# Kernel tuning notes

Hardware: AMD Instinct MI355X
Metric: run time of the kernel (lower is better)

Reference implementation:

```python
import jax, jax.numpy as jnp
import numpy as np

N = 100            # node_num
B = 8              # batch
H = 256            # node_feature_hidden_dim
FD, FL = 16, 16    # node_feature_dim, node_feature_len
OUT = 4            # edge_output_dim
E = N * (N - 1)    # 9900 directed edges (off-diagonal)
_off = np.ones((N, N)) - np.eye(N)
REC, SEND = np.where(_off)   # rel_rec one-hot rows = REC, rel_send = SEND
REC = jnp.asarray(REC, jnp.int32)
SEND = jnp.asarray(SEND, jnp.int32)
BN_EPS = 1e-5


def _mlp(x, w1, b1, w2, b2, g, beta):
    # Linear-ReLU-Linear-ReLU-BatchNorm1d (training-mode batch stats, dropout=0)
    h = jax.nn.relu(x @ w1 + b1)
    h = jax.nn.relu(h @ w2 + b2)
    b_, e_, f_ = h.shape
    hf = h.reshape(b_ * e_, f_)
    mu = hf.mean(0)
    var = hf.var(0)  # biased variance, as torch BN uses for normalization
    hn = (hf - mu) * jax.lax.rsqrt(var + BN_EPS) * g + beta
    return hn.reshape(b_, e_, f_)


def _node2edge(x):
    # gather form of rel_send @ x / rel_rec @ x, cat([senders, receivers])
    return jnp.concatenate([x[:, SEND, :], x[:, REC, :]], axis=2)


def _edge2node(x):
    # scatter form of rel_rec.T @ x; original divides by incoming.size(1) == N
    incoming = jnp.zeros((x.shape[0], N, x.shape[2]), x.dtype).at[:, REC, :].add(x)
    return incoming / N


def setup_inputs() -> dict:
    key = jax.random.key(0)
    ks = jax.random.split(key, 40)

    def rn(k, shape, s=0.05):
        return (jax.random.normal(k, shape) * s).astype(jnp.float32)

    inp = {
        'x': rn(ks[0], (B, N, FD, FL), 1.0),
        'h': rn(ks[1], (B, N, 8, 8), 1.0),
        't_nodes': N,
        't_edges': E,
        'nodes_mask': jnp.ones((N,), jnp.int32),
        'edges_mask': jnp.ones((E,), jnp.int32),
    }
    n_in = {'mlp1': FD * FL, 'mlp2': 2 * H, 'mlp3': H, 'mlp4': 3 * H}
    i = 2
    for name, nin in n_in.items():
        inp[name + '_w1'] = rn(ks[i], (nin, H)); i += 1
        inp[name + '_b1'] = jnp.full((H,), 0.1, jnp.float32)
        inp[name + '_w2'] = rn(ks[i], (H, H)); i += 1
        inp[name + '_b2'] = jnp.full((H,), 0.1, jnp.float32)
        inp[name + '_g'] = jnp.ones((H,), jnp.float32)
        inp[name + '_beta'] = jnp.zeros((H,), jnp.float32)
    inp['fc_w'] = rn(ks[i], (H, OUT)); i += 1
    inp['fc_b'] = jnp.full((OUT,), 0.1, jnp.float32)
    return inp


def reference(x, h, t_nodes, t_edges, nodes_mask, edges_mask,
              mlp1_w1, mlp1_b1, mlp1_w2, mlp1_b2, mlp1_g, mlp1_beta,
              mlp2_w1, mlp2_b1, mlp2_w2, mlp2_b2, mlp2_g, mlp2_beta,
              mlp3_w1, mlp3_b1, mlp3_w2, mlp3_b2, mlp3_g, mlp3_beta,
              mlp4_w1, mlp4_b1, mlp4_w2, mlp4_b2, mlp4_g, mlp4_beta,
              fc_w, fc_b):
    # h, t_nodes, t_edges, nodes_mask, edges_mask are unused by the original forward
    xx = x.reshape(x.shape[0], x.shape[1], -1).astype(jnp.float32)  # [B,N,FD*FL]
    xx = _mlp(xx, mlp1_w1, mlp1_b1, mlp1_w2, mlp1_b2, mlp1_g, mlp1_beta)  # [B,N,H]
    xe = _node2edge(xx)                                                   # [B,E,2H]
    xe = _mlp(xe, mlp2_w1, mlp2_b1, mlp2_w2, mlp2_b2, mlp2_g, mlp2_beta)  # [B,E,H]
    x_skip = xe
    xn = _edge2node(xe)                                                   # [B,N,H]
    xn = _mlp(xn, mlp3_w1, mlp3_b1, mlp3_w2, mlp3_b2, mlp3_g, mlp3_beta)
    xe2 = _node2edge(xn)                                                  # [B,E,2H]
    xc = jnp.concatenate([xe2, x_skip], axis=2)                           # [B,E,3H]
    xc = _mlp(xc, mlp4_w1, mlp4_b1, mlp4_w2, mlp4_b2, mlp4_g, mlp4_beta)  # [B,E,H]
    z_g = xc @ fc_w + fc_b                                                # [B,E,OUT]
    return z_g
```

## Files before the change

kernel.cpp:

```cpp
#include <hip/hip_runtime.h>
#include <hip/hip_bf16.h>

#define Nn 100
#define Bb 8
#define Hh 256
#define Ee 9900
#define RE 79200
#define RN 800
#define BN_EPS 1e-5f

typedef __attribute__((ext_vector_type(8))) unsigned short ushort8_t;
typedef __attribute__((ext_vector_type(4))) unsigned short ushort4_t;
typedef __attribute__((ext_vector_type(8))) short bf16x8;
typedef __attribute__((ext_vector_type(4))) float f32x4;

__device__ __forceinline__ float bf2f(unsigned short u){
  return __uint_as_float(((unsigned)u) << 16);
}
__device__ __forceinline__ unsigned short f2bf(float f){
  unsigned u = __float_as_uint(f);
  return (unsigned short)((u + 0x7fffu + ((u >> 16) & 1u)) >> 16);
}

__device__ __forceinline__ void affine_prologue(const float* __restrict__ stats,
    float cnt, const float* __restrict__ g, const float* __restrict__ beta,
    float* a, float* c, int tid){
  if (tid < 256){
    float inv = 1.0f / cnt;
    float mu  = stats[tid] * inv;
    float var = fmaxf(stats[256 + tid] * inv - mu * mu, 0.f);
    float aa  = g[tid] * rsqrtf(var + BN_EPS);
    a[tid] = aa;
    c[tid] = beta[tid] - mu * aa;
  }
}

__device__ __forceinline__ void affine_reg(const float* __restrict__ stats,
    float cnt, const float* __restrict__ g, const float* __restrict__ be,
    int cb, float4& av, float4& cv){
  float4 s = *(const float4*)(stats + cb);
  float4 q = *(const float4*)(stats + 256 + cb);
  float4 gg = *(const float4*)(g + cb);
  float4 bb = *(const float4*)(be + cb);
  float inv = 1.0f / cnt;
  float mx = s.x*inv, my = s.y*inv, mz = s.z*inv, mw = s.w*inv;
  av.x = gg.x * rsqrtf(fmaxf(q.x*inv - mx*mx, 0.f) + BN_EPS); cv.x = bb.x - mx*av.x;
  av.y = gg.y * rsqrtf(fmaxf(q.y*inv - my*my, 0.f) + BN_EPS); cv.y = bb.y - my*av.y;
  av.z = gg.z * rsqrtf(fmaxf(q.z*inv - mz*mz, 0.f) + BN_EPS); cv.z = bb.z - mz*av.z;
  av.w = gg.w * rsqrtf(fmaxf(q.w*inv - mw*mw, 0.f) + BN_EPS); cv.w = bb.w - mw*av.w;
}

__device__ __forceinline__ void gemm_f32(const float* IN, const float* __restrict__ W,
                                         float acc[8][4], int tr, int tc){
  for (int k = 0; k < 256; k += 4){
    float4 w0 = *(const float4*)(W + (size_t)(k+0)*256 + 4*tc);
    float4 w1 = *(const float4*)(W + (size_t)(k+1)*256 + 4*tc);
    float4 w2 = *(const float4*)(W + (size_t)(k+2)*256 + 4*tc);
    float4 w3 = *(const float4*)(W + (size_t)(k+3)*256 + 4*tc);
    #pragma unroll
    for (int rr = 0; rr < 8; rr++){
      float4 iv = *(const float4*)(IN + (tr*8+rr)*256 + k);
      acc[rr][0] += iv.x*w0.x + iv.y*w1.x + iv.z*w2.x + iv.w*w3.x;
      acc[rr][1] += iv.x*w0.y + iv.y*w1.y + iv.z*w2.y + iv.w*w3.y;
      acc[rr][2] += iv.x*w0.z + iv.y*w1.z + iv.z*w2.z + iv.w*w3.z;
      acc[rr][3] += iv.x*w0.w + iv.y*w1.w + iv.z*w2.w + iv.w*w3.w;
    }
  }
}

template<int KW>
__device__ __forceinline__ void mfma_gemm(const unsigned short* Alds,
    const unsigned short* __restrict__ Bf, f32x4 acc[2][4], int w, int lane){
  const int l15 = lane & 15, kg = lane >> 4;
  for (int ks = 0; ks < KW/32; ks++){
    int byte0 = ((l15*KW      + ks*32 + kg*8) * 2) ^ ((l15 & 7) << 4);
    int byte1 = (((16+l15)*KW + ks*32 + kg*8) * 2) ^ ((l15 & 7) << 4);
    bf16x8 a0 = *(const bf16x8*)((const char*)Alds + byte0);
    bf16x8 a1 = *(const bf16x8*)((const char*)Alds + byte1);
    const unsigned short* bp = Bf + ((size_t)(ks*16 + w*4)*64 + lane)*8;
    #pragma unroll
    for (int cf = 0; cf < 4; cf++){
      bf16x8 b = *(const bf16x8*)(bp + cf*64*8);
      acc[0][cf] = __builtin_amdgcn_mfma_f32_16x16x32_bf16(a0, b, acc[0][cf], 0,0,0);
      acc[1][cf] = __builtin_amdgcn_mfma_f32_16x16x32_bf16(a1, b, acc[1][cf], 0,0,0);
    }
  }
}

__device__ __forceinline__ void zero_acc(f32x4 acc[2][4]){
  #pragma unroll
  for (int i = 0; i < 2; i++)
    #pragma unroll
    for (int j = 0; j < 4; j++){
      f32x4 z = {0.f, 0.f, 0.f, 0.f};
      acc[i][j] = z;
    }
}

#define STATS_PUSH(statsp)                                   \
  __syncthreads();                                           \
  atomicAdd(&(statsp)[tid], red[tid]);                       \
  atomicAdd(&(statsp)[tid + 256], red[tid + 256]);

__global__ void k_wprep(const float* __restrict__ W, unsigned short* __restrict__ out,
                        int ktiles){
  int id = blockIdx.x * 256 + threadIdx.x;
  int total = ktiles * 16 * 64;
  if (id >= total) return;
  int lane = id & 63, tile = id >> 6;
  int tc = tile & 15, tk = tile >> 4;
  int kbase = tk*32 + (lane>>4)*8, col = tc*16 + (lane&15);
  ushort8_t o;
  #pragma unroll
  for (int j = 0; j < 8; j++) o[j] = f2bf(W[(size_t)(kbase+j)*256 + col]);
  *(ushort8_t*)(out + (size_t)id*8) = o;
}

__global__ __launch_bounds__(256,2) void k_mlp1(
    const float* __restrict__ x,
    const float* __restrict__ W1, const float* __restrict__ b1,
    const float* __restrict__ W2, const float* __restrict__ b2,
    float* __restrict__ h1, float* __restrict__ stats){
  __shared__ float IN[32*256];
  __shared__ float O1[32*256];
  __shared__ float red[512];
  int tid = threadIdx.x, tr = tid >> 6, tc = tid & 63;
  int r0 = blockIdx.x * 32;
  #pragma unroll
  for (int j = 0; j < 8; j++){
    int idx = tid*4 + j*1024;
    *(float4*)(IN + idx) = *(const float4*)(x + (size_t)r0*256 + idx);
  }
  red[tid] = 0.f; red[tid + 256] = 0.f;
  __syncthreads();
  float acc[8][4];
  #pragma unroll
  for (int rr = 0; rr < 8; rr++){ acc[rr][0]=acc[rr][1]=acc[rr][2]=acc[rr][3]=0.f; }
  gemm_f32(IN, W1, acc, tr, tc);
  {
    float4 bb = *(const float4*)(b1 + 4*tc);
    #pragma unroll
    for (int rr = 0; rr < 8; rr++){
      float4 o;
      o.x = fmaxf(acc[rr][0]+bb.x, 0.f);
      o.y = fmaxf(acc[rr][1]+bb.y, 0.f);
      o.z = fmaxf(acc[rr][2]+bb.z, 0.f);
      o.w = fmaxf(acc[rr][3]+bb.w, 0.f);
      *(float4*)(O1 + (tr*8+rr)*256 + 4*tc) = o;
    }
  }
  __syncthreads();
  #pragma unroll
  for (int rr = 0; rr < 8; rr++){ acc[rr][0]=acc[rr][1]=acc[rr][2]=acc[rr][3]=0.f; }
  gemm_f32(O1, W2, acc, tr, tc);
  {
    float4 bb = *(const float4*)(b2 + 4*tc);
    float ls0=0,ls1=0,ls2=0,ls3=0,lq0=0,lq1=0,lq2=0,lq3=0;
    #pragma unroll
    for (int rr = 0; rr < 8; rr++){
      float4 v;
      v.x = fmaxf(acc[rr][0]+bb.x, 0.f);
      v.y = fmaxf(acc[rr][1]+bb.y, 0.f);
      v.z = fmaxf(acc[rr][2]+bb.z, 0.f);
      v.w = fmaxf(acc[rr][3]+bb.w, 0.f);
      *(float4*)(h1 + ((size_t)(r0 + tr*8 + rr))*256 + 4*tc) = v;
      ls0+=v.x; lq0+=v.x*v.x; ls1+=v.y; lq1+=v.y*v.y;
      ls2+=v.z; lq2+=v.z*v.z; ls3+=v.w; lq3+=v.w*v.w;
    }
    atomicAdd(&red[4*tc+0], ls0); atomicAdd(&red[4*tc+1], ls1);
    atomicAdd(&red[4*tc+2], ls2); atomicAdd(&red[4*tc+3], ls3);
    atomicAdd(&red[256+4*tc+0], lq0); atomicAdd(&red[256+4*tc+1], lq1);
    atomicAdd(&red[256+4*tc+2], lq2); atomicAdd(&red[256+4*tc+3], lq3);
  }
  STATS_PUSH(stats)
}

__global__ __launch_bounds__(256,2) void k_nodepq(
    const float* __restrict__ hsrc, const float* __restrict__ stats,
    const float* __restrict__ g, const float* __restrict__ be,
    const float* __restrict__ W512,
    float* __restrict__ P, float* __restrict__ Q){
  __shared__ float IN[32*256];
  int tid = threadIdx.x, tr = tid >> 6, tc = tid & 63;
  int part = blockIdx.x / 25;
  int r0 = (blockIdx.x % 25) * 32;
  int cb = (tid*4) & 255;
  float4 av, cv;
  affine_reg(stats, (float)RN, g, be, cb, av, cv);
  #pragma unroll
  for (int j = 0; j < 8; j++){
    int idx = tid*4 + j*1024;
    int row = idx >> 8;
    float4 v = *(const float4*)(hsrc + (size_t)(r0+row)*256 + cb);
    float4 o;
    o.x = v.x*av.x + cv.x; o.y = v.y*av.y + cv.y;
    o.z = v.z*av.z + cv.z; o.w = v.w*av.w + cv.w;
    *(float4*)(IN + idx) = o;
  }
  __syncthreads();
  float acc[8][4];
  #pragma unroll
  for (int rr = 0; rr < 8; rr++){ acc[rr][0]=acc[rr][1]=acc[rr][2]=acc[rr][3]=0.f; }
  gemm_f32(IN, W512 + (size_t)part*65536, acc, tr, tc);
  float* out = part ? Q : P;
  #pragma unroll
  for (int rr = 0; rr < 8; rr++){
    float4 o; o.x=acc[rr][0]; o.y=acc[rr][1]; o.z=acc[rr][2]; o.w=acc[rr][3];
    *(float4*)(out + (size_t)(r0 + tr*8 + rr)*256 + 4*tc) = o;
  }
}

__global__ __launch_bounds__(256,6) void k_mlp2(
    const float* __restrict__ P2, const float* __restrict__ Q2,
    const float* __restrict__ b1,
    const unsigned short* __restrict__ W2f, const float* __restrict__ b2,
    unsigned short* __restrict__ h2, float* __restrict__ stats2){
  __shared__ unsigned short O1[32*256];
  __shared__ float red[512];
  int tid = threadIdx.x, w = tid >> 6, lane = tid & 63;
  int l15 = lane & 15, kg = lane >> 4;
  int r0 = blockIdx.x * 32;
  red[tid] = 0.f; red[tid + 256] = 0.f;
  {
    int cb = lane * 4;
    float4 bb = *(const float4*)(b1 + cb);
    #pragma unroll
    for (int rr = 0; rr < 8; rr++){
      int rl = w*8+rr, rg = r0 + rl;
      int b = rg / Ee, e = rg - b*Ee;
      int i = e / 99, kk = e - i*99;
      int snd = kk + (kk >= i);
      float4 pv = *(const float4*)(P2 + ((size_t)(b*Nn + snd))*256 + cb);
      float4 qv = *(const float4*)(Q2 + ((size_t)(b*Nn + i))*256 + cb);
      ushort4_t o;
      o[0] = f2bf(fmaxf(pv.x+qv.x+bb.x, 0.f));
      o[1] = f2bf(fmaxf(pv.y+qv.y+bb.y, 0.f));
      o[2] = f2bf(fmaxf(pv.z+qv.z+bb.z, 0.f));
      o[3] = f2bf(fmaxf(pv.w+qv.w+bb.w, 0.f));
      int byte = ((rl*256 + cb)*2) ^ ((rl&7)<<4);
      *(ushort4_t*)((char*)O1 + byte) = o;
    }
  }
  __syncthreads();
  f32x4 acc2[2][4];
  zero_acc(acc2);
  mfma_gemm<256>(O1, W2f, acc2, w, lane);
  {
    #pragma unroll
    for (int cf = 0; cf < 4; cf++){
      int col = w*64 + cf*16 + l15;
      float bb = b2[col];
      float ls = 0.f, lq = 0.f;
      #pragma unroll
      for (int rf = 0; rf < 2; rf++){
        #pragma unroll
        for (int r = 0; r < 4; r++){
          int row = rf*16 + kg*4 + r;
          float v = fmaxf(acc2[rf][cf][r] + bb, 0.f);
          h2[(size_t)(r0 + row)*256 + col] = f2bf(v);
          ls += v; lq += v*v;
        }
      }
      atomicAdd(&red[col], ls);
      atomicAdd(&red[256+col], lq);
    }
  }
  STATS_PUSH(stats2)
}

__global__ __launch_bounds__(256,4) void k_e2n(
    const unsigned short* __restrict__ h2, float* __restrict__ h3in){
  int m = blockIdx.x;
  int b = m / Nn, i = m - b*Nn;
  int c = threadIdx.x;
  const unsigned short* base = h2 + ((size_t)(b*Ee + i*99))*256 + c;
  float s = 0.f;
  #pragma unroll 4
  for (int j = 0; j < 99; j++) s += bf2f(base[(size_t)j*256]);
  h3in[(size_t)m*256 + c] = s;
}

__global__ __launch_bounds__(256,2) void k_mlp3(
    const float* __restrict__ h3in, const float* __restrict__ stats2,
    const float* __restrict__ g2, const float* __restrict__ be2,
    const float* __restrict__ W1, const float* __restrict__ b1,
    const float* __restrict__ W2, const float* __restrict__ b2,
    float* __restrict__ h3, float* __restrict__ stats3){
  __shared__ float IN[32*256];
  __shared__ float O1[32*256];
  __shared__ float red[512];
  __shared__ float ap[256], cp[256];
  int tid = threadIdx.x, tr = tid >> 6, lane = tid & 63, tc = lane;
  int r0 = blockIdx.x * 32;
  affine_prologue(stats2, (float)RE, g2, be2, ap, cp, tid);
  red[tid] = 0.f; red[tid + 256] = 0.f;
  __syncthreads();
  {
    int cb = lane * 4;
    float4 av = *(const float4*)(ap+cb), cv = *(const float4*)(cp+cb);
    #pragma unroll
    for (int rr = 0; rr < 8; rr++){
      int m = r0 + tr*8 + rr;
      float4 s = *(const float4*)(h3in + (size_t)m*256 + cb);
      float4 o;
      o.x = (s.x*av.x + 99.f*cv.x) * 0.01f;
      o.y = (s.y*av.y + 99.f*cv.y) * 0.01f;
      o.z = (s.z*av.z + 99.f*cv.z) * 0.01f;
      o.w = (s.w*av.w + 99.f*cv.w) * 0.01f;
      *(float4*)(IN + (tr*8+rr)*256 + cb) = o;
    }
  }
  __syncthreads();
  float acc[8][4];
  #pragma unroll
  for (int rr = 0; rr < 8; rr++){ acc[rr][0]=acc[rr][1]=acc[rr][2]=acc[rr][3]=0.f; }
  gemm_f32(IN, W1, acc, tr, tc);
  {
    float4 bb = *(const float4*)(b1 + 4*tc);
    #pragma unroll
    for (int rr = 0; rr < 8; rr++){
      float4 o;
      o.x = fmaxf(acc[rr][0]+bb.x, 0.f);
      o.y = fmaxf(acc[rr][1]+bb.y, 0.f);
      o.z = fmaxf(acc[rr][2]+bb.z, 0.f);
      o.w = fmaxf(acc[rr][3]+bb.w, 0.f);
      *(float4*)(O1 + (tr*8+rr)*256 + 4*tc) = o;
    }
  }
  __syncthreads();
  #pragma unroll
  for (int rr = 0; rr < 8; rr++){ acc[rr][0]=acc[rr][1]=acc[rr][2]=acc[rr][3]=0.f; }
  gemm_f32(O1, W2, acc, tr, tc);
  {
    float4 bb = *(const float4*)(b2 + 4*tc);
    float ls0=0,ls1=0,ls2=0,ls3=0,lq0=0,lq1=0,lq2=0,lq3=0;
    #pragma unroll
    for (int rr = 0; rr < 8; rr++){
      float4 v;
      v.x = fmaxf(acc[rr][0]+bb.x, 0.f);
      v.y = fmaxf(acc[rr][1]+bb.y, 0.f);
      v.z = fmaxf(acc[rr][2]+bb.z, 0.f);
      v.w = fmaxf(acc[rr][3]+bb.w, 0.f);
      *(float4*)(h3 + ((size_t)(r0 + tr*8 + rr))*256 + 4*tc) = v;
      ls0+=v.x; lq0+=v.x*v.x; ls1+=v.y; lq1+=v.y*v.y;
      ls2+=v.z; lq2+=v.z*v.z; ls3+=v.w; lq3+=v.w*v.w;
    }
    atomicAdd(&red[4*tc+0], ls0); atomicAdd(&red[4*tc+1], ls1);
    atomicAdd(&red[4*tc+2], ls2); atomicAdd(&red[4*tc+3], ls3);
    atomicAdd(&red[256+4*tc+0], lq0); atomicAdd(&red[256+4*tc+1], lq1);
    atomicAdd(&red[256+4*tc+2], lq2); atomicAdd(&red[256+4*tc+3], lq3);
  }
  STATS_PUSH(stats3)
}

__global__ __launch_bounds__(256,6) void k_mlp4(
    const unsigned short* __restrict__ h2,
    const float* __restrict__ stats2, const float* __restrict__ g2, const float* __restrict__ be2,
    const float* __restrict__ P4, const float* __restrict__ Q4,
    const float* __restrict__ b1,
    const unsigned short* __restrict__ Wsf,
    const unsigned short* __restrict__ W2f, const float* __restrict__ b2,
    unsigned short* __restrict__ h4, float* __restrict__ stats4){
  __shared__ unsigned short A[32*256];
  __shared__ float red[512];
  __shared__ int sIdx[32], rIdx[32];
  int tid = threadIdx.x, w = tid >> 6, lane = tid & 63;
  int l15 = lane & 15, kg = lane >> 4;
  int r0 = blockIdx.x * 32;
  red[tid] = 0.f; red[tid + 256] = 0.f;
  if (tid < 32){
    int rg = r0 + tid;
    int b = rg / Ee, e = rg - b*Ee;
    int i = e / 99, kk = e - i*99;
    int snd = kk + (kk >= i);
    sIdx[tid] = (b*Nn + snd)*256;
    rIdx[tid] = (b*Nn + i)*256;
  }
  {
    int cb = lane * 4;
    float4 av, cv;
    affine_reg(stats2, (float)RE, g2, be2, cb, av, cv);
    #pragma unroll
    for (int rr = 0; rr < 8; rr++){
      int rl = w*8+rr, rg = r0 + rl;
      ushort4_t hv = *(const ushort4_t*)(h2 + (size_t)rg*256 + cb);
      ushort4_t o;
      o[0]=f2bf(bf2f(hv[0])*av.x+cv.x);
      o[1]=f2bf(bf2f(hv[1])*av.y+cv.y);
      o[2]=f2bf(bf2f(hv[2])*av.z+cv.z);
      o[3]=f2bf(bf2f(hv[3])*av.w+cv.w);
      int byte = ((rl*256 + cb)*2) ^ ((rl&7)<<4);
      *(ushort4_t*)((char*)A + byte) = o;
    }
  }
  __syncthreads();
  f32x4 acc[2][4];
  zero_acc(acc);
  mfma_gemm<256>(A, Wsf, acc, w, lane);
  __syncthreads();
  unsigned short* O1 = A;
  {
    #pragma unroll
    for (int cf = 0; cf < 4; cf++){
      int col = w*64 + cf*16 + l15;
      float bb = b1[col];
      #pragma unroll
      for (int rf = 0; rf < 2; rf++){
        #pragma unroll
        for (int r = 0; r < 4; r++){
          int row = rf*16 + kg*4 + r;
          float v = acc[rf][cf][r] + P4[sIdx[row] + col] + Q4[rIdx[row] + col] + bb;
          v = fmaxf(v, 0.f);
          int byte = ((row*256 + col)*2) ^ ((row&7)<<4);
          *(unsigned short*)((char*)O1 + byte) = f2bf(v);
        }
      }
    }
  }
  __syncthreads();
  f32x4 acc2[2][4];
  zero_acc(acc2);
  mfma_gemm<256>(O1, W2f, acc2, w, lane);
  {
    #pragma unroll
    for (int cf = 0; cf < 4; cf++){
      int col = w*64 + cf*16 + l15;
      float bb = b2[col];
      float ls = 0.f, lq = 0.f;
      #pragma unroll
      for (int rf = 0; rf < 2; rf++){
        #pragma unroll
        for (int r = 0; r < 4; r++){
          int row = rf*16 + kg*4 + r;
          float v = fmaxf(acc2[rf][cf][r] + bb, 0.f);
          h4[(size_t)(r0 + row)*256 + col] = f2bf(v);
          ls += v; lq += v*v;
        }
      }
      atomicAdd(&red[col], ls);
      atomicAdd(&red[256+col], lq);
    }
  }
  STATS_PUSH(stats4)
}

__global__ __launch_bounds__(256,2) void k_out(
    const unsigned short* __restrict__ h4, const float* __restrict__ stats4,
    const float* __restrict__ g4, const float* __restrict__ be4,
    const float* __restrict__ fcw, const float* __restrict__ fcb,
    float* __restrict__ out){
  __shared__ unsigned short T[64*264];
  __shared__ float a4[256], c4[256], Wl[1024];
  int tid = threadIdx.x;
  affine_prologue(stats4, (float)RE, g4, be4, a4, c4, tid);
  #pragma unroll
  for (int j = 0; j < 4; j++){ int id = tid + j*256; Wl[id] = fcw[id]; }
  int r0 = blockIdx.x * 64;
  #pragma unroll
  for (int j = 0; j < 8; j++){
    int flat = tid + j*256;
    int rl = flat >> 5, cs = (flat & 31) * 8;
    ushort8_t v = {0,0,0,0,0,0,0,0};
    if (r0 + rl < RE) v = *(const ushort8_t*)(h4 + (size_t)(r0+rl)*256 + cs);
    *(ushort8_t*)(&T[rl*264 + cs]) = v;
  }
  __syncthreads();
  int row = tid >> 2, o = tid & 3;
  if (r0 + row < RE){
    float acc = fcb[o];
    for (int k = 0; k < 256; k += 8){
      ushort8_t iv = *(const ushort8_t*)(&T[row*264 + k]);
      #pragma unroll
      for (int kk = 0; kk < 8; kk++){
        float v = bf2f(iv[kk]) * a4[k+kk] + c4[k+kk];
        acc += v * Wl[(k+kk)*4 + o];
      }
    }
    out[(size_t)(r0+row)*4 + o] = acc;
  }
}

extern "C" void kernel_launch(void* const* d_in, const int* in_sizes, int n_in,
                              void* d_out, int out_size, void* d_ws, size_t ws_size,
                              hipStream_t stream){
  const float* x    = (const float*)d_in[0];
  const float* m1w1 = (const float*)d_in[6];  const float* m1b1 = (const float*)d_in[7];
  const float* m1w2 = (const float*)d_in[8];  const float* m1b2 = (const float*)d_in[9];
  const float* m1g  = (const float*)d_in[10]; const float* m1be = (const float*)d_in[11];
  const float* m2w1 = (const float*)d_in[12]; const float* m2b1 = (const float*)d_in[13];
  const float* m2w2 = (const float*)d_in[14]; const float* m2b2 = (const float*)d_in[15];
  const float* m2g  = (const float*)d_in[16]; const float* m2be = (const float*)d_in[17];
  const float* m3w1 = (const float*)d_in[18]; const float* m3b1 = (const float*)d_in[19];
  const float* m3w2 = (const float*)d_in[20]; const float* m3b2 = (const float*)d_in[21];
  const float* m3g  = (const float*)d_in[22]; const float* m3be = (const float*)d_in[23];
  const float* m4w1 = (const float*)d_in[24]; const float* m4b1 = (const float*)d_in[25];
  const float* m4w2 = (const float*)d_in[26]; const float* m4b2 = (const float*)d_in[27];
  const float* m4g  = (const float*)d_in[28]; const float* m4be = (const float*)d_in[29];
  const float* fcw  = (const float*)d_in[30]; const float* fcb  = (const float*)d_in[31];

  size_t need_bytes = 1435648ull * 4ull
                    + (2ull * (size_t)RE * 256ull + 3ull * 65536ull) * 2ull;
  if (ws_size < need_bytes) return;

  float* ws = (float*)d_ws;
  float* h1   = ws;
  float* h3   = ws + 204800;
  float* stats= ws + 409600;
  float* h3in = ws + 411648;
  float* P2   = ws + 616448;
  float* Q2   = ws + 821248;
  float* P4   = ws + 1026048;
  float* Q4   = ws + 1230848;
  unsigned short* h2  = (unsigned short*)(ws + 1435648);
  unsigned short* h4  = h2 + (size_t)RE * 256;
  unsigned short* w2b = h4 + (size_t)RE * 256;
  unsigned short* w4s = w2b + 65536;
  unsigned short* w4b = w4s + 65536;

  hipMemsetAsync(stats, 0, 2048 * sizeof(float), stream);

  k_wprep<<<(8*16*64)/256, 256, 0, stream>>>(m2w2, w2b, 8);
  k_wprep<<<(8*16*64)/256, 256, 0, stream>>>(m4w1 + (size_t)512*256, w4s, 8);
  k_wprep<<<(8*16*64)/256, 256, 0, stream>>>(m4w2, w4b, 8);

  k_mlp1<<<RN/32, 256, 0, stream>>>(x, m1w1, m1b1, m1w2, m1b2, h1, stats);
  k_nodepq<<<50, 256, 0, stream>>>(h1, stats, m1g, m1be, m2w1, P2, Q2);
  k_mlp2<<<RE/32, 256, 0, stream>>>(P2, Q2, m2b1, w2b, m2b2, h2, stats + 512);
  k_e2n<<<RN, 256, 0, stream>>>(h2, h3in);
  k_mlp3<<<RN/32, 256, 0, stream>>>(h3in, stats + 512, m2g, m2be,
                                    m3w1, m3b1, m3w2, m3b2, h3, stats + 1024);
  k_nodepq<<<50, 256, 0, stream>>>(h3, stats + 1024, m3g, m3be, m4w1, P4, Q4);
  k_mlp4<<<RE/32, 256, 0, stream>>>(h2, stats + 512, m2g, m2be,
                                    P4, Q4, m4b1, w4s, w4b, m4b2, h4, stats + 1536);
  k_out<<<(RE+63)/64, 256, 0, stream>>>(h4, stats + 1536, m4g, m4be,
                                        fcw, fcb, (float*)d_out);
}
```

Before: 513.9 us.

## Use 64-row edge tiles in MFMA kernels and store node projections in bf16

The edge MLP kernels (mlp2, mlp4) now process 64 rows per block instead of 32, so each weight fragment loaded from global memory feeds four MFMA row-fragments rather than two. Tail rows are clamped on load and skipped on store. The node projections P/Q are also stored as bf16 instead of fp32, which halves the gather traffic in the edge kernels. In exchange, register and LDS use go up (launch bounds drop to 4 blocks), the grid shrinks, and there is a small loss of precision on P/Q.

```diff
diff --git a/kernel.cpp b/kernel.cpp
--- a/kernel.cpp
+++ b/kernel.cpp
@@ -68,28 +68,30 @@
   }
 }
 
-template<int KW>
-__device__ __forceinline__ void mfma_gemm(const unsigned short* Alds,
-    const unsigned short* __restrict__ Bf, f32x4 acc[2][4], int w, int lane){
+__device__ __forceinline__ void mfma_gemm64(const unsigned short* Alds,
+    const unsigned short* __restrict__ Bf, f32x4 acc[4][4], int w, int lane){
   const int l15 = lane & 15, kg = lane >> 4;
-  for (int ks = 0; ks < KW/32; ks++){
-    int byte0 = ((l15*KW      + ks*32 + kg*8) * 2) ^ ((l15 & 7) << 4);
-    int byte1 = (((16+l15)*KW + ks*32 + kg*8) * 2) ^ ((l15 & 7) << 4);
-    bf16x8 a0 = *(const bf16x8*)((const char*)Alds + byte0);
-    bf16x8 a1 = *(const bf16x8*)((const char*)Alds + byte1);
+  for (int ks = 0; ks < 8; ks++){
+    bf16x8 a[4];
+    #pragma unroll
+    for (int rf = 0; rf < 4; rf++){
+      int byte = (((rf*16 + l15)*256 + ks*32 + kg*8) * 2) ^ ((l15 & 7) << 4);
+      a[rf] = *(const bf16x8*)((const char*)Alds + byte);
+    }
     const unsigned short* bp = Bf + ((size_t)(ks*16 + w*4)*64 + lane)*8;
     #pragma unroll
     for (int cf = 0; cf < 4; cf++){
       bf16x8 b = *(const bf16x8*)(bp + cf*64*8);
-      acc[0][cf] = __builtin_amdgcn_mfma_f32_16x16x32_bf16(a0, b, acc[0][cf], 0,0,0);
-      acc[1][cf] = __builtin_amdgcn_mfma_f32_16x16x32_bf16(a1, b, acc[1][cf], 0,0,0);
-    }
-  }
-}
-
-__device__ __forceinline__ void zero_acc(f32x4 acc[2][4]){
-  #pragma unroll
-  for (int i = 0; i < 2; i++)
+      #pragma unroll
+      for (int rf = 0; rf < 4; rf++)
+        acc[rf][cf] = __builtin_amdgcn_mfma_f32_16x16x32_bf16(a[rf], b, acc[rf][cf], 0,0,0);
+    }
+  }
+}
+
+__device__ __forceinline__ void zero_acc4(f32x4 acc[4][4]){
+  #pragma unroll
+  for (int i = 0; i < 4; i++)
     #pragma unroll
     for (int j = 0; j < 4; j++){
       f32x4 z = {0.f, 0.f, 0.f, 0.f};
@@ -179,7 +181,7 @@
     const float* __restrict__ hsrc, const float* __restrict__ stats,
     const float* __restrict__ g, const float* __restrict__ be,
     const float* __restrict__ W512,
-    float* __restrict__ P, float* __restrict__ Q){
+    unsigned short* __restrict__ P, unsigned short* __restrict__ Q){
   __shared__ float IN[32*256];
   int tid = threadIdx.x, tr = tid >> 6, tc = tid & 63;
   int part = blockIdx.x / 25;
@@ -202,49 +204,52 @@
   #pragma unroll
   for (int rr = 0; rr < 8; rr++){ acc[rr][0]=acc[rr][1]=acc[rr][2]=acc[rr][3]=0.f; }
   gemm_f32(IN, W512 + (size_t)part*65536, acc, tr, tc);
-  float* out = part ? Q : P;
+  unsigned short* out = part ? Q : P;
   #pragma unroll
   for (int rr = 0; rr < 8; rr++){
-    float4 o; o.x=acc[rr][0]; o.y=acc[rr][1]; o.z=acc[rr][2]; o.w=acc[rr][3];
-    *(float4*)(out + (size_t)(r0 + tr*8 + rr)*256 + 4*tc) = o;
-  }
-}
-
-__global__ __launch_bounds__(256,6) void k_mlp2(
-    const float* __restrict__ P2, const float* __restrict__ Q2,
+    ushort4_t o;
+    o[0]=f2bf(acc[rr][0]); o[1]=f2bf(acc[rr][1]);
+    o[2]=f2bf(acc[rr][2]); o[3]=f2bf(acc[rr][3]);
+    *(ushort4_t*)(out + (size_t)(r0 + tr*8 + rr)*256 + 4*tc) = o;
+  }
+}
+
+__global__ __launch_bounds__(256,4) void k_mlp2(
+    const unsigned short* __restrict__ P2, const unsigned short* __restrict__ Q2,
     const float* __restrict__ b1,
     const unsigned short* __restrict__ W2f, const float* __restrict__ b2,
     unsigned short* __restrict__ h2, float* __restrict__ stats2){
-  __shared__ unsigned short O1[32*256];
+  __shared__ unsigned short O1[64*256];
   __shared__ float red[512];
   int tid = threadIdx.x, w = tid >> 6, lane = tid & 63;
   int l15 = lane & 15, kg = lane >> 4;
-  int r0 = blockIdx.x * 32;
+  int r0 = blockIdx.x * 64;
   red[tid] = 0.f; red[tid + 256] = 0.f;
   {
     int cb = lane * 4;
     float4 bb = *(const float4*)(b1 + cb);
     #pragma unroll
-    for (int rr = 0; rr < 8; rr++){
-      int rl = w*8+rr, rg = r0 + rl;
-      int b = rg / Ee, e = rg - b*Ee;
+    for (int rr = 0; rr < 16; rr++){
+      int rl = w*16+rr, rg = r0 + rl;
+      int rgc = rg < RE ? rg : RE-1;
+      int b = rgc / Ee, e = rgc - b*Ee;
       int i = e / 99, kk = e - i*99;
       int snd = kk + (kk >= i);
-      float4 pv = *(const float4*)(P2 + ((size_t)(b*Nn + snd))*256 + cb);
-      float4 qv = *(const float4*)(Q2 + ((size_t)(b*Nn + i))*256 + cb);
+      ushort4_t pv = *(const ushort4_t*)(P2 + ((size_t)(b*Nn + snd))*256 + cb);
+      ushort4_t qv = *(const ushort4_t*)(Q2 + ((size_t)(b*Nn + i))*256 + cb);
       ushort4_t o;
-      o[0] = f2bf(fmaxf(pv.x+qv.x+bb.x, 0.f));
-      o[1] = f2bf(fmaxf(pv.y+qv.y+bb.y, 0.f));
-      o[2] = f2bf(fmaxf(pv.z+qv.z+bb.z, 0.f));
-      o[3] = f2bf(fmaxf(pv.w+qv.w+bb.w, 0.f));
+      o[0] = f2bf(fmaxf(bf2f(pv[0])+bf2f(qv[0])+bb.x, 0.f));
+      o[1] = f2bf(fmaxf(bf2f(pv[1])+bf2f(qv[1])+bb.y, 0.f));
+      o[2] = f2bf(fmaxf(bf2f(pv[2])+bf2f(qv[2])+bb.z, 0.f));
+      o[3] = f2bf(fmaxf(bf2f(pv[3])+bf2f(qv[3])+bb.w, 0.f));
       int byte = ((rl*256 + cb)*2) ^ ((rl&7)<<4);
       *(ushort4_t*)((char*)O1 + byte) = o;
     }
   }
   __syncthreads();
-  f32x4 acc2[2][4];
-  zero_acc(acc2);
-  mfma_gemm<256>(O1, W2f, acc2, w, lane);
+  f32x4 acc2[4][4];
+  zero_acc4(acc2);
+  mfma_gemm64(O1, W2f, acc2, w, lane);
   {
     #pragma unroll
     for (int cf = 0; cf < 4; cf++){
@@ -252,13 +257,15 @@
       float bb = b2[col];
       float ls = 0.f, lq = 0.f;
       #pragma unroll
-      for (int rf = 0; rf < 2; rf++){
+      for (int rf = 0; rf < 4; rf++){
         #pragma unroll
         for (int r = 0; r < 4; r++){
           int row = rf*16 + kg*4 + r;
-          float v = fmaxf(acc2[rf][cf][r] + bb, 0.f);
-          h2[(size_t)(r0 + row)*256 + col] = f2bf(v);
-          ls += v; lq += v*v;
+          if (r0 + row < RE){
+            float v = fmaxf(acc2[rf][cf][r] + bb, 0.f);
+            h2[(size_t)(r0 + row)*256 + col] = f2bf(v);
+            ls += v; lq += v*v;
+          }
         }
       }
       atomicAdd(&red[col], ls);
@@ -353,24 +360,25 @@
   STATS_PUSH(stats3)
 }
 
-__global__ __launch_bounds__(256,6) void k_mlp4(
+__global__ __launch_bounds__(256,4) void k_mlp4(
     const unsigned short* __restrict__ h2,
     const float* __restrict__ stats2, const float* __restrict__ g2, const float* __restrict__ be2,
-    const float* __restrict__ P4, const float* __restrict__ Q4,
+    const unsigned short* __restrict__ P4, const unsigned short* __restrict__ Q4,
     const float* __restrict__ b1,
     const unsigned short* __restrict__ Wsf,
     const unsigned short* __restrict__ W2f, const float* __restrict__ b2,
     unsigned short* __restrict__ h4, float* __restrict__ stats4){
-  __shared__ unsigned short A[32*256];
+  __shared__ unsigned short A[64*256];
   __shared__ float red[512];
-  __shared__ int sIdx[32], rIdx[32];
+  __shared__ int sIdx[64], rIdx[64];
   int tid = threadIdx.x, w = tid >> 6, lane = tid & 63;
   int l15 = lane & 15, kg = lane >> 4;
-  int r0 = blockIdx.x * 32;
+  int r0 = blockIdx.x * 64;
   red[tid] = 0.f; red[tid + 256] = 0.f;
-  if (tid < 32){
+  if (tid < 64){
     int rg = r0 + tid;
-    int b = rg / Ee, e = rg - b*Ee;
+    int rgc = rg < RE ? rg : RE-1;
+    int b = rgc / Ee, e = rgc - b*Ee;
     int i = e / 99, kk = e - i*99;
     int snd = kk + (kk >= i);
     sIdx[tid] = (b*Nn + snd)*256;
@@ -381,9 +389,10 @@
     float4 av, cv;
     affine_reg(stats2, (float)RE, g2, be2, cb, av, cv);
     #pragma unroll
-    for (int rr = 0; rr < 8; rr++){
-      int rl = w*8+rr, rg = r0 + rl;
-      ushort4_t hv = *(const ushort4_t*)(h2 + (size_t)rg*256 + cb);
+    for (int rr = 0; rr < 16; rr++){
+      int rl = w*16+rr, rg = r0 + rl;
+      int rgc = rg < RE ? rg : RE-1;
+      ushort4_t hv = *(const ushort4_t*)(h2 + (size_t)rgc*256 + cb);
       ushort4_t o;
       o[0]=f2bf(bf2f(hv[0])*av.x+cv.x);
       o[1]=f2bf(bf2f(hv[1])*av.y+cv.y);
@@ -394,9 +403,9 @@
     }
   }
   __syncthreads();
-  f32x4 acc[2][4];
-  zero_acc(acc);
-  mfma_gemm<256>(A, Wsf, acc, w, lane);
+  f32x4 acc[4][4];
+  zero_acc4(acc);
+  mfma_gemm64(A, Wsf, acc, w, lane);
   __syncthreads();
   unsigned short* O1 = A;
   {
@@ -405,11 +414,11 @@
       int col = w*64 + cf*16 + l15;
       float bb = b1[col];
       #pragma unroll
-      for (int rf = 0; rf < 2; rf++){
+      for (int rf = 0; rf < 4; rf++){
         #pragma unroll
         for (int r = 0; r < 4; r++){
           int row = rf*16 + kg*4 + r;
-          float v = acc[rf][cf][r] + P4[sIdx[row] + col] + Q4[rIdx[row] + col] + bb;
+          float v = acc[rf][cf][r] + bf2f(P4[sIdx[row] + col]) + bf2f(Q4[rIdx[row] + col]) + bb;
           v = fmaxf(v, 0.f);
           int byte = ((row*256 + col)*2) ^ ((row&7)<<4);
           *(unsigned short*)((char*)O1 + byte) = f2bf(v);
@@ -418,9 +427,9 @@
     }
   }
   __syncthreads();
-  f32x4 acc2[2][4];
-  zero_acc(acc2);
-  mfma_gemm<256>(O1, W2f, acc2, w, lane);
+  f32x4 acc2[4][4];
+  zero_acc4(acc2);
+  mfma_gemm64(O1, W2f, acc2, w, lane);
   {
     #pragma unroll
     for (int cf = 0; cf < 4; cf++){
@@ -428,13 +437,15 @@
       float bb = b2[col];
       float ls = 0.f, lq = 0.f;
       #pragma unroll
-      for (int rf = 0; rf < 2; rf++){
+      for (int rf = 0; rf < 4; rf++){
         #pragma unroll
         for (int r = 0; r < 4; r++){
           int row = rf*16 + kg*4 + r;
-          float v = fmaxf(acc2[rf][cf][r] + bb, 0.f);
-          h4[(size_t)(r0 + row)*256 + col] = f2bf(v);
-          ls += v; lq += v*v;
+          if (r0 + row < RE){
+            float v = fmaxf(acc2[rf][cf][r] + bb, 0.f);
+            h4[(size_t)(r0 + row)*256 + col] = f2bf(v);
+            ls += v; lq += v*v;
+          }
         }
       }
       atomicAdd(&red[col], ls);
@@ -498,8 +509,8 @@
   const float* m4g  = (const float*)d_in[28]; const float* m4be = (const float*)d_in[29];
   const float* fcw  = (const float*)d_in[30]; const float* fcb  = (const float*)d_in[31];
 
-  size_t need_bytes = 1435648ull * 4ull
-                    + (2ull * (size_t)RE * 256ull + 3ull * 65536ull) * 2ull;
+  size_t need_bytes = 616448ull * 4ull
+                    + (2ull * (size_t)RE * 256ull + 3ull * 65536ull + 4ull * 204800ull) * 2ull;
   if (ws_size < need_bytes) return;
 
   float* ws = (float*)d_ws;
@@ -507,15 +518,15 @@
   float* h3   = ws + 204800;
   float* stats= ws + 409600;
   float* h3in = ws + 411648;
-  float* P2   = ws + 616448;
-  float* Q2   = ws + 821248;
-  float* P4   = ws + 1026048;
-  float* Q4   = ws + 1230848;
-  unsigned short* h2  = (unsigned short*)(ws + 1435648);
+  unsigned short* h2  = (unsigned short*)(ws + 616448);
   unsigned short* h4  = h2 + (size_t)RE * 256;
   unsigned short* w2b = h4 + (size_t)RE * 256;
   unsigned short* w4s = w2b + 65536;
   unsigned short* w4b = w4s + 65536;
+  unsigned short* P2b = w4b + 65536;
+  unsigned short* Q2b = P2b + 204800;
+  unsigned short* P4b = Q2b + 204800;
+  unsigned short* Q4b = P4b + 204800;
 
   hipMemsetAsync(stats, 0, 2048 * sizeof(float), stream);
 
@@ -524,14 +535,14 @@
   k_wprep<<<(8*16*64)/256, 256, 0, stream>>>(m4w2, w4b, 8);
 
   k_mlp1<<<RN/32, 256, 0, stream>>>(x, m1w1, m1b1, m1w2, m1b2, h1, stats);
-  k_nodepq<<<50, 256, 0, stream>>>(h1, stats, m1g, m1be, m2w1, P2, Q2);
-  k_mlp2<<<RE/32, 256, 0, stream>>>(P2, Q2, m2b1, w2b, m2b2, h2, stats + 512);
+  k_nodepq<<<50, 256, 0, stream>>>(h1, stats, m1g, m1be, m2w1, P2b, Q2b);
+  k_mlp2<<<(RE+63)/64, 256, 0, stream>>>(P2b, Q2b, m2b1, w2b, m2b2, h2, stats + 512);
   k_e2n<<<RN, 256, 0, stream>>>(h2, h3in);
   k_mlp3<<<RN/32, 256, 0, stream>>>(h3in, stats + 512, m2g, m2be,
                                     m3w1, m3b1, m3w2, m3b2, h3, stats + 1024);
-  k_nodepq<<<50, 256, 0, stream>>>(h3, stats + 1024, m3g, m3be, m4w1, P4, Q4);
-  k_mlp4<<<RE/32, 256, 0, stream>>>(h2, stats + 512, m2g, m2be,
-                                    P4, Q4, m4b1, w4s, w4b, m4b2, h4, stats + 1536);
+  k_nodepq<<<50, 256, 0, stream>>>(h3, stats + 1024, m3g, m3be, m4w1, P4b, Q4b);
+  k_mlp4<<<(RE+63)/64, 256, 0, stream>>>(h2, stats + 512, m2g, m2be,
+                                         P4b, Q4b, m4b1, w4s, w4b, m4b2, h4, stats + 1536);
   k_out<<<(RE+63)/64, 256, 0, stream>>>(h4, stats + 1536, m4g, m4be,
                                         fcw, fcb, (float*)d_out);
 }
```

Result: no change. 504.7 us (-1.8%).
